# Optimization experiments

Measured on AMD Instinct MI355X. Metric: run time of the kernel, lower is better.

Reference implementation:

```python
import jax, jax.numpy as jnp
import numpy as np

B, N, D_IN, D_EMB = 8, 2048, 768, 768

def setup_inputs() -> dict:
    key = jax.random.key(0)
    k1, k2, k3, k4 = jax.random.split(key, 4)
    x = jax.random.normal(k1, (B, N, D_IN), dtype=jnp.float32)
    # nn.Linear weights stored as [out, in]; applied as x @ W.T
    Wq = jax.random.normal(k2, (D_EMB, D_IN), dtype=jnp.float32) * (D_IN ** -0.5)
    Wk = jax.random.normal(k3, (D_EMB, D_IN), dtype=jnp.float32) * (D_IN ** -0.5)
    Wv = jax.random.normal(k4, (D_EMB, D_IN), dtype=jnp.float32) * (D_IN ** -0.5)
    return {"x": x, "Wq": Wq, "Wk": Wk, "Wv": Wv}

def reference(x, Wq, Wk, Wv):
    dim_sqrt = jnp.asarray(D_EMB ** 0.5, x.dtype)
    q = jnp.einsum('bnd,ed->bne', x, Wq)  # [B,N,E]
    k = jnp.einsum('bnd,ed->bne', x, Wk)
    v = jnp.einsum('bnd,ed->bne', x, Wv)
    scores = jnp.einsum('bne,bme->bnm', q, k)  # [B,N,N]
    # NOTE: module applies softmax FIRST, then divides by sqrt(d) (post-hoc)
    attn = jax.nn.softmax(scores, axis=-1) / dim_sqrt
    out = jnp.einsum('bnm,bme->bne', attn, v)
    return out
```

## Files before the change

### kernel.cpp

```cpp
#include <hip/hip_runtime.h>
#include <stdint.h>
#include <type_traits>

typedef __bf16 bf16;
typedef _Float16 f16;
typedef bf16 bf16x8 __attribute__((ext_vector_type(8)));
typedef f16 f16x8 __attribute__((ext_vector_type(8)));
typedef float f32x4 __attribute__((ext_vector_type(4)));

#define LOG2E 1.4426950408889634f
#define SQRT_E 27.712812921102035f

constexpr int BM = 128, BN = 128, BK = 64;
enum { EPI_F32 = 0, EPI_PAIR = 1, EPI_VT = 2, EPI_F16 = 3 };

__device__ __forceinline__ void async16(const void* g, void* l) {
  __builtin_amdgcn_global_load_lds(
      (__attribute__((address_space(1))) void*)(uintptr_t)g,
      (__attribute__((address_space(3))) void*)l, 16, 0, 0);
}

__device__ __forceinline__ f32x4 mfma8(bf16x8 a, bf16x8 b, f32x4 c) {
  return __builtin_amdgcn_mfma_f32_16x16x32_bf16(a, b, c, 0, 0, 0);
}
__device__ __forceinline__ f32x4 mfma8(f16x8 a, f16x8 b, f32x4 c) {
  return __builtin_amdgcn_mfma_f32_16x16x32_f16(a, b, c, 0, 0, 0);
}

template <typename T, typename TO, int AT, int BT, int EPI, int SWZ>
__global__ __launch_bounds__(256)
void gemm_kernel(const T* __restrict__ Ah, const T* __restrict__ Al,
                 const T* __restrict__ Bh, const T* __restrict__ Bl,
                 void* __restrict__ C0, void* __restrict__ C1,
                 int K, long lda, long ldb, long ldbl, long ldc,
                 long stA, long stB, long stBl, long stC,
                 int gxN, int gyM) {
  using vec8 = typename std::conditional<std::is_same<T, bf16>::value,
                                         bf16x8, f16x8>::type;
  __shared__ __align__(16) T sAh[BM * BK];
  __shared__ __align__(16) T sBh[BN * BK];
  __shared__ __align__(16) T sAl[AT == 2 ? BM * BK : 8];
  __shared__ __align__(16) T sBl[BT == 2 ? BN * BK : 8];

  int bxi, byi, z;
  if constexpr (SWZ) {
    const int id = blockIdx.x;
    const int xcd = id & 7;
    const int j = id >> 3;
    const int s = j / gxN;
    const int n = j - s * gxN;
    const int g = xcd + 8 * s;
    bxi = n;
    byi = g % gyM;
    z = g / gyM;
  } else {
    bxi = blockIdx.x; byi = blockIdx.y; z = blockIdx.z;
  }

  const T* pAh = Ah + (long)z * stA;
  const T* pBh = Bh + (long)z * stB;
  const T* pAl = (AT == 2) ? (Al + (long)z * stA) : nullptr;
  const T* pBl = (BT == 2) ? (Bl + (long)z * stBl) : nullptr;

  const int bm = byi * BM;
  const int bn = bxi * BN;
  const int tid = threadIdx.x;
  const int wave = tid >> 6;
  const int lane = tid & 63;
  const int wm = (wave & 1) * 64;
  const int wn = (wave >> 1) * 64;
  const int quad = lane >> 4;
  const int l16 = lane & 15;

  f32x4 acc[4][4] = {};

  const int sr0 = tid >> 3;
  const int swc = ((tid & 7) ^ (sr0 & 7)) * 8;
  const int cs0 = (quad * 8) ^ ((l16 & 7) << 3);

  for (int kt = 0; kt < K; kt += BK) {
    __syncthreads();
    {
      const long ka = kt + swc;
#pragma unroll
      for (int l = 0; l < 4; ++l) {
        const int row = l * 32 + sr0;
        async16(pAh + (long)(bm + row) * lda + ka, &sAh[(l * 256 + tid) * 8]);
      }
#pragma unroll
      for (int l = 0; l < 4; ++l) {
        const int row = l * 32 + sr0;
        async16(pBh + (long)(bn + row) * ldb + ka, &sBh[(l * 256 + tid) * 8]);
      }
      if constexpr (AT == 2) {
#pragma unroll
        for (int l = 0; l < 4; ++l) {
          const int row = l * 32 + sr0;
          async16(pAl + (long)(bm + row) * lda + ka, &sAl[(l * 256 + tid) * 8]);
        }
      }
      if constexpr (BT == 2) {
#pragma unroll
        for (int l = 0; l < 4; ++l) {
          const int row = l * 32 + sr0;
          async16(pBl + (long)(bn + row) * ldbl + ka, &sBl[(l * 256 + tid) * 8]);
        }
      }
    }
    __syncthreads();

#pragma unroll
    for (int kk = 0; kk < 2; ++kk) {
      const int cs = cs0 ^ (kk * 32);
      vec8 ah[4], al[4];
#pragma unroll
      for (int i = 0; i < 4; ++i) {
        ah[i] = *(const vec8*)&sAh[(wm + i * 16 + l16) * BK + cs];
        if constexpr (AT == 2)
          al[i] = *(const vec8*)&sAl[(wm + i * 16 + l16) * BK + cs];
      }
#pragma unroll
      for (int j = 0; j < 4; ++j) {
        const vec8 bh = *(const vec8*)&sBh[(wn + j * 16 + l16) * BK + cs];
        vec8 bl;
        if constexpr (BT == 2)
          bl = *(const vec8*)&sBl[(wn + j * 16 + l16) * BK + cs];
#pragma unroll
        for (int i = 0; i < 4; ++i) {
          acc[i][j] = mfma8(ah[i], bh, acc[i][j]);
          if constexpr (BT == 2) acc[i][j] = mfma8(ah[i], bl, acc[i][j]);
          if constexpr (AT == 2) acc[i][j] = mfma8(al[i], bh, acc[i][j]);
        }
      }
    }
  }

  if constexpr (EPI == EPI_F32) {
    float* C = (float*)C0 + (long)z * stC;
#pragma unroll
    for (int i = 0; i < 4; ++i) {
      const int mb = bm + wm + i * 16 + quad * 4;
#pragma unroll
      for (int j = 0; j < 4; ++j) {
        const int n = bn + wn + j * 16 + l16;
#pragma unroll
        for (int r = 0; r < 4; ++r)
          C[(long)(mb + r) * ldc + n] = acc[i][j][r];
      }
    }
  } else if constexpr (EPI == EPI_PAIR) {
    TO* Ch = (TO*)C0;
    TO* Cl = (TO*)C1;
#pragma unroll
    for (int i = 0; i < 4; ++i) {
      const int mb = bm + wm + i * 16 + quad * 4;
#pragma unroll
      for (int j = 0; j < 4; ++j) {
        const int n = bn + wn + j * 16 + l16;
#pragma unroll
        for (int r = 0; r < 4; ++r) {
          const float f = acc[i][j][r];
          const TO h = (TO)f;
          const long idx = (long)(mb + r) * ldc + n;
          Ch[idx] = h;
          Cl[idx] = (TO)(f - (float)h);
        }
      }
    }
  } else if constexpr (EPI == EPI_F16) {
    TO* Ch = (TO*)C0;
#pragma unroll
    for (int i = 0; i < 4; ++i) {
      const int mb = bm + wm + i * 16 + quad * 4;
#pragma unroll
      for (int j = 0; j < 4; ++j) {
        const int n = bn + wn + j * 16 + l16;
#pragma unroll
        for (int r = 0; r < 4; ++r)
          Ch[(long)(mb + r) * ldc + n] = (TO)acc[i][j][r];
      }
    }
  } else {
    TO* vT = (TO*)C0;
#pragma unroll
    for (int i = 0; i < 4; ++i) {
      const int mb = bm + wm + i * 16 + quad * 4;
      const long bb = mb >> 11;
      const long ml = mb & 2047;
#pragma unroll
      for (int j = 0; j < 4; ++j) {
        const int e = bn + wn + j * 16 + l16;
        union { TO b[4]; uint2 u; } P;
#pragma unroll
        for (int r = 0; r < 4; ++r) P.b[r] = (TO)acc[i][j][r];
        *(uint2*)&vT[(bb * 768 + e) * 2048 + ml] = P.u;
      }
    }
  }
}

__global__ __launch_bounds__(256)
void softmax_kernel(float* __restrict__ sc) {
  __shared__ float red[4];
  float* srow = sc + (long)blockIdx.x * 2048;
  const int tid = threadIdx.x;
  const int wave = tid >> 6;
  const int lane = tid & 63;
  const float4 v0 = *(const float4*)(srow + tid * 4);
  const float4 v1 = *(const float4*)(srow + 1024 + tid * 4);
  float mx = fmaxf(fmaxf(fmaxf(v0.x, v0.y), fmaxf(v0.z, v0.w)),
                   fmaxf(fmaxf(v1.x, v1.y), fmaxf(v1.z, v1.w)));
#pragma unroll
  for (int o = 32; o >= 1; o >>= 1) mx = fmaxf(mx, __shfl_xor(mx, o));
  if (lane == 0) red[wave] = mx;
  __syncthreads();
  mx = fmaxf(fmaxf(red[0], red[1]), fmaxf(red[2], red[3]));
  const float e0 = exp2f((v0.x - mx) * LOG2E);
  const float e1 = exp2f((v0.y - mx) * LOG2E);
  const float e2 = exp2f((v0.z - mx) * LOG2E);
  const float e3 = exp2f((v0.w - mx) * LOG2E);
  const float e4 = exp2f((v1.x - mx) * LOG2E);
  const float e5 = exp2f((v1.y - mx) * LOG2E);
  const float e6 = exp2f((v1.z - mx) * LOG2E);
  const float e7 = exp2f((v1.w - mx) * LOG2E);
  float s = ((e0 + e1) + (e2 + e3)) + ((e4 + e5) + (e6 + e7));
#pragma unroll
  for (int o = 32; o >= 1; o >>= 1) s += __shfl_xor(s, o);
  __syncthreads();
  if (lane == 0) red[wave] = s;
  __syncthreads();
  s = red[0] + red[1] + red[2] + red[3];
  const float inv = 1.0f / (s * SQRT_E);
  f16* prow = (f16*)srow;
  union { f16 b[4]; uint2 u; } P;
  P.b[0] = (f16)(e0 * inv); P.b[1] = (f16)(e1 * inv);
  P.b[2] = (f16)(e2 * inv); P.b[3] = (f16)(e3 * inv);
  *(uint2*)(prow + tid * 4) = P.u;
  P.b[0] = (f16)(e4 * inv); P.b[1] = (f16)(e5 * inv);
  P.b[2] = (f16)(e6 * inv); P.b[3] = (f16)(e7 * inv);
  *(uint2*)(prow + 1024 + tid * 4) = P.u;
}

__global__ __launch_bounds__(256)
void split_all(const float4* __restrict__ x, const float4* __restrict__ wv,
               uint2* __restrict__ xh, uint2* __restrict__ xl,
               uint2* __restrict__ wvh) {
  constexpr int NX = 3145728;
  constexpr int NWV = 147456;
  const int i = blockIdx.x * 256 + threadIdx.x;
  float4 v;
  uint2 *dh, *dl;
  if (i < NX) {
    v = x[i]; dh = xh + i; dl = xl + i;
  } else {
    const int m = i - NX;
    if (m >= NWV) return;
    v = wv[m]; dh = wvh + m; dl = nullptr;
  }
  const f16 h0 = (f16)v.x, h1 = (f16)v.y, h2 = (f16)v.z, h3 = (f16)v.w;
  union { f16 b[4]; uint2 u; } P;
  P.b[0] = h0; P.b[1] = h1; P.b[2] = h2; P.b[3] = h3;
  *dh = P.u;
  if (dl != nullptr) {
    P.b[0] = (f16)(v.x - (float)h0);
    P.b[1] = (f16)(v.y - (float)h1);
    P.b[2] = (f16)(v.z - (float)h2);
    P.b[3] = (f16)(v.w - (float)h3);
    *dl = P.u;
  }
}

__global__ __launch_bounds__(256)
void transpose_split(const float* __restrict__ Wq, const float* __restrict__ Wk,
                     f16* __restrict__ qTh, f16* __restrict__ qTl,
                     f16* __restrict__ kTh, f16* __restrict__ kTl) {
  __shared__ float tile[64][65];
  const float* src = blockIdx.z ? Wk : Wq;
  f16* dh = blockIdx.z ? kTh : qTh;
  f16* dl = blockIdx.z ? kTl : qTl;
  const int e0 = blockIdx.y * 64, d0 = blockIdx.x * 64;
  const int t = threadIdx.x;
  const int r = t >> 2;
  const int c4 = (t & 3) * 16;
  const float4* s4 = (const float4*)(src + (long)(e0 + r) * 768 + d0 + c4);
#pragma unroll
  for (int g = 0; g < 4; ++g) {
    const float4 v = s4[g];
    tile[r][c4 + g * 4 + 0] = v.x;
    tile[r][c4 + g * 4 + 1] = v.y;
    tile[r][c4 + g * 4 + 2] = v.z;
    tile[r][c4 + g * 4 + 3] = v.w;
  }
  __syncthreads();
  union { f16 b[8]; uint4 u; } H0, H1, L0, L1;
#pragma unroll
  for (int i = 0; i < 16; ++i) {
    const float v = tile[c4 + i][r];
    const f16 h = (f16)v;
    const f16 l = (f16)(v - (float)h);
    if (i < 8) { H0.b[i] = h; L0.b[i] = l; }
    else       { H1.b[i - 8] = h; L1.b[i - 8] = l; }
  }
  const long o = (long)(d0 + r) * 768 + e0 + c4;
  *(uint4*)(dh + o) = H0.u;  *(uint4*)(dh + o + 8) = H1.u;
  *(uint4*)(dl + o) = L0.u;  *(uint4*)(dl + o + 8) = L1.u;
}

extern "C" void kernel_launch(void* const* d_in, const int* in_sizes, int n_in,
                              void* d_out, int out_size, void* d_ws, size_t ws_size,
                              hipStream_t stream) {
  const float* x  = (const float*)d_in[0];
  const float* Wq = (const float*)d_in[1];
  const float* Wk = (const float*)d_in[2];
  const float* Wv = (const float*)d_in[3];
  float* out = (float*)d_out;
  char* ws = (char*)d_ws;

  const size_t SZ = 25165824;
  f16* yh = (f16*)(ws + 0 * SZ);
  f16* xh = (f16*)(ws + 2 * SZ);
  f16* vT = (f16*)(ws + 3 * SZ);
  const size_t PERS = 4 * SZ;
  const size_t WT = 1179648;
  f16* xl   = (f16*)(ws + PERS);
  f16* wqTh = (f16*)(ws + PERS + SZ);
  f16* wqTl = (f16*)(ws + PERS + SZ + 1 * WT);
  f16* wkTh = (f16*)(ws + PERS + SZ + 2 * WT);
  f16* wkTl = (f16*)(ws + PERS + SZ + 3 * WT);
  f16* mtH  = (f16*)(ws + PERS + SZ + 4 * WT);
  f16* mtL  = (f16*)(ws + PERS + SZ + 5 * WT);
  f16* wvh  = (f16*)(ws + PERS + SZ + 6 * WT);
  float* scores = (float*)(ws + PERS);

  long avail = (long)ws_size - (long)PERS;
  int nb = (int)(avail / 16777216);
  if (nb < 1) nb = 1;
  if (nb > 8) nb = 8;

  split_all<<<12864, 256, 0, stream>>>(
      (const float4*)x, (const float4*)Wv, (uint2*)xh, (uint2*)xl, (uint2*)wvh);
  transpose_split<<<dim3(12, 12, 2), 256, 0, stream>>>(
      Wq, Wk, wqTh, wqTl, wkTh, wkTl);

  gemm_kernel<f16, f16, 2, 2, EPI_PAIR, 0><<<dim3(6, 6, 1), 256, 0, stream>>>(
      wkTh, wkTl, wqTh, wqTl, (void*)mtH, (void*)mtL,
      768, 768, 768, 768, 768, 0, 0, 0, 0, 0, 0);

  gemm_kernel<f16, f16, 2, 1, EPI_F16, 1><<<768, 256, 0, stream>>>(
      xh, xl, mtH, nullptr, (void*)yh, nullptr,
      768, 768, 768, 0, 768, 0, 0, 0, 0, 6, 128);

  gemm_kernel<f16, f16, 1, 1, EPI_VT, 1><<<768, 256, 0, stream>>>(
      xh, nullptr, wvh, nullptr, (void*)vT, nullptr,
      768, 768, 768, 0, 0, 0, 0, 0, 0, 6, 128);

  const long RS = 1572864;
  const long VTS = 1572864;
  for (int b0 = 0; b0 < 8; b0 += nb) {
    const int nbg = (8 - b0 < nb) ? (8 - b0) : nb;
    gemm_kernel<f16, float, 1, 1, EPI_F32, 1><<<256 * nbg, 256, 0, stream>>>(
        yh + (long)b0 * RS, nullptr, xh + (long)b0 * RS, nullptr,
        (void*)scores, nullptr,
        768, 768, 768, 0, 2048, RS, RS, 0, 4194304L, 16, 16);
    softmax_kernel<<<nbg * 2048, 256, 0, stream>>>(scores);
    gemm_kernel<f16, float, 1, 1, EPI_F32, 1><<<96 * nbg, 256, 0, stream>>>(
        (const f16*)scores, nullptr, vT + (long)b0 * VTS, nullptr,
        (void*)(out + (long)b0 * 1572864), nullptr,
        2048, 4096, 2048, 0, 768, 8388608L, VTS, 0, 1572864L, 6, 16);
  }
}
```

Baseline: 370.1 us.

## Add double-buffered pipelined GEMM kernel with larger tiles for attention stages

Introduces a new gemm_pipe kernel that double-buffers LDS tiles, issuing async global-to-LDS loads for the next K-tile while computing the current one, with explicit vmcnt waits, MFMA priority hints and an XCD-aware block mapping. The score GEMM moves to 256x256 tiles with 512 threads, and the projection GEMMs use the pipelined path, one of them with BK=32. The goal is to hide global load latency and raise reuse per tile. In exchange it doubles LDS use, which may lower occupancy, and it relies on hand-tuned waitcnt logic.

```diff
diff --git a/kernel.cpp b/kernel.cpp
--- a/kernel.cpp
+++ b/kernel.cpp
@@ -11,7 +11,6 @@
 #define LOG2E 1.4426950408889634f
 #define SQRT_E 27.712812921102035f
 
-constexpr int BM = 128, BN = 128, BK = 64;
 enum { EPI_F32 = 0, EPI_PAIR = 1, EPI_VT = 2, EPI_F16 = 3 };
 
 __device__ __forceinline__ void async16(const void* g, void* l) {
@@ -26,6 +25,199 @@
 __device__ __forceinline__ f32x4 mfma8(f16x8 a, f16x8 b, f32x4 c) {
   return __builtin_amdgcn_mfma_f32_16x16x32_f16(a, b, c, 0, 0, 0);
 }
+
+template <int N>
+__device__ __forceinline__ void vwait() {
+  asm volatile("s_waitcnt vmcnt(%0)" ::"i"(N) : "memory");
+}
+__device__ __forceinline__ void block_bar() {
+  asm volatile("" ::: "memory");
+  __builtin_amdgcn_s_barrier();
+  asm volatile("" ::: "memory");
+}
+
+template <typename T, typename TO, int BMt, int BNt, int BKt, int AT, int EPI>
+__global__ __launch_bounds__((BMt == 256 ? 512 : 256), 2)
+void gemm_pipe(const T* __restrict__ Ah, const T* __restrict__ Al,
+               const T* __restrict__ Bh, void* __restrict__ C0,
+               int K, long lda, long ldb, long ldc,
+               long stA, long stB, long stC, int gxN, int gyM) {
+  using vec8 = typename std::conditional<std::is_same<T, bf16>::value,
+                                         bf16x8, f16x8>::type;
+  static_assert(BMt == BNt, "square tiles only");
+  constexpr int THREADS = (BMt == 256) ? 512 : 256;
+  constexpr int NWN = (BMt == 256) ? 4 : 2;
+  constexpr int WTM = BMt / 2;
+  constexpr int WTN = BNt / NWN;
+  static_assert(WTN == 64, "wave tile must be 64 wide");
+  constexpr int MF = WTM / 16;
+  constexpr int KK = BKt / 32;
+  constexpr int CPR = BKt / 8;
+  constexpr int RPI = THREADS / CPR;
+  constexpr int LPP = (BMt * BKt) / (THREADS * 8);
+  constexpr int LPT = LPP * (AT == 2 ? 3 : 2);
+
+  __shared__ __align__(16) T sA[2][BMt * BKt];
+  __shared__ __align__(16) T sB[2][BNt * BKt];
+  __shared__ __align__(16) T sAl[AT == 2 ? 2 * BMt * BKt : 8];
+
+  const int id = blockIdx.x;
+  const int xcd = id & 7;
+  const int j0 = id >> 3;
+  const int s = j0 / gxN;
+  const int bxi = j0 - s * gxN;
+  const int g = xcd + 8 * s;
+  const int byi = g % gyM;
+  const int z = g / gyM;
+
+  const T* pA = Ah + (long)z * stA;
+  const T* pB = Bh + (long)z * stB;
+  const T* pAl = (AT == 2) ? Al : nullptr;
+
+  const int bm = byi * BMt;
+  const int bn = bxi * BNt;
+  const int tid = threadIdx.x;
+  const int wave = tid >> 6;
+  const int lane = tid & 63;
+  const int wm = (wave / NWN) * WTM;
+  const int wn = (wave % NWN) * WTN;
+  const int quad = lane >> 4;
+  const int l16 = lane & 15;
+
+  f32x4 acc[MF][4] = {};
+
+  const int srow = tid / CPR;
+  const int schk = tid % CPR;
+  const int swc = ((BKt == 64) ? (schk ^ (srow & 7)) : schk) * 8;
+  const int cs0 = (quad * 8) ^ ((BKt == 64) ? ((l16 & 7) << 3) : 0);
+
+  const int NT = K / BKt;
+
+  auto stage = [&](int buf, int t) {
+    const long ka = (long)t * BKt + swc;
+#pragma unroll
+    for (int l = 0; l < LPP; ++l)
+      async16(pA + (long)(bm + l * RPI + srow) * lda + ka,
+              &sA[buf][(l * THREADS + tid) * 8]);
+#pragma unroll
+    for (int l = 0; l < LPP; ++l)
+      async16(pB + (long)(bn + l * RPI + srow) * ldb + ka,
+              &sB[buf][(l * THREADS + tid) * 8]);
+    if constexpr (AT == 2) {
+#pragma unroll
+      for (int l = 0; l < LPP; ++l)
+        async16(pAl + (long)(bm + l * RPI + srow) * lda + ka,
+                &sAl[buf * BMt * BKt + (l * THREADS + tid) * 8]);
+    }
+  };
+
+  auto compute = [&](int buf) {
+    const T* bA = &sA[buf][0];
+    const T* bB = &sB[buf][0];
+    const T* bAl = (AT == 2) ? &sAl[buf * BMt * BKt] : nullptr;
+    vec8 bf[KK][4];
+#pragma unroll
+    for (int kk = 0; kk < KK; ++kk)
+#pragma unroll
+      for (int jj = 0; jj < 4; ++jj)
+        bf[kk][jj] =
+            *(const vec8*)&bB[(wn + jj * 16 + l16) * BKt + (cs0 ^ (kk * 32))];
+#pragma unroll
+    for (int mq = 0; mq < MF / 2; ++mq) {
+      vec8 af[KK][2];
+      vec8 alf[AT == 2 ? KK : 1][2];
+#pragma unroll
+      for (int kk = 0; kk < KK; ++kk)
+#pragma unroll
+        for (int ii = 0; ii < 2; ++ii) {
+          const int r = wm + mq * 32 + ii * 16 + l16;
+          af[kk][ii] = *(const vec8*)&bA[r * BKt + (cs0 ^ (kk * 32))];
+          if constexpr (AT == 2)
+            alf[kk][ii] = *(const vec8*)&bAl[r * BKt + (cs0 ^ (kk * 32))];
+        }
+      __builtin_amdgcn_s_setprio(1);
+#pragma unroll
+      for (int jj = 0; jj < 4; ++jj)
+#pragma unroll
+        for (int ii = 0; ii < 2; ++ii)
+#pragma unroll
+          for (int kk = 0; kk < KK; ++kk) {
+            acc[mq * 2 + ii][jj] =
+                mfma8(af[kk][ii], bf[kk][jj], acc[mq * 2 + ii][jj]);
+            if constexpr (AT == 2)
+              acc[mq * 2 + ii][jj] =
+                  mfma8(alf[kk][ii], bf[kk][jj], acc[mq * 2 + ii][jj]);
+          }
+      __builtin_amdgcn_s_setprio(0);
+    }
+  };
+
+  stage(0, 0);
+  stage(1, 1);
+  vwait<LPT>();
+  block_bar();
+
+  for (int t = 0; t < NT; ++t) {
+    const int cur = t & 1;
+    compute(cur);
+    if (t + 1 < NT) {
+      block_bar();
+      if (t + 2 < NT) {
+        stage(cur, t + 2);
+        vwait<LPT>();
+      } else {
+        vwait<0>();
+      }
+      block_bar();
+    }
+  }
+
+  if constexpr (EPI == EPI_F32) {
+    float* C = (float*)C0 + (long)z * stC;
+#pragma unroll
+    for (int i = 0; i < MF; ++i) {
+      const int mb = bm + wm + i * 16 + quad * 4;
+#pragma unroll
+      for (int j = 0; j < 4; ++j) {
+        const int n = bn + wn + j * 16 + l16;
+#pragma unroll
+        for (int r = 0; r < 4; ++r)
+          C[(long)(mb + r) * ldc + n] = acc[i][j][r];
+      }
+    }
+  } else if constexpr (EPI == EPI_F16) {
+    TO* Ch = (TO*)C0;
+#pragma unroll
+    for (int i = 0; i < MF; ++i) {
+      const int mb = bm + wm + i * 16 + quad * 4;
+#pragma unroll
+      for (int j = 0; j < 4; ++j) {
+        const int n = bn + wn + j * 16 + l16;
+#pragma unroll
+        for (int r = 0; r < 4; ++r)
+          Ch[(long)(mb + r) * ldc + n] = (TO)acc[i][j][r];
+      }
+    }
+  } else {
+    TO* vT = (TO*)C0;
+#pragma unroll
+    for (int i = 0; i < MF; ++i) {
+      const int mb = bm + wm + i * 16 + quad * 4;
+      const long bb = mb >> 11;
+      const long ml = mb & 2047;
+#pragma unroll
+      for (int j = 0; j < 4; ++j) {
+        const int e = bn + wn + j * 16 + l16;
+        union { TO b[4]; uint2 u; } P;
+#pragma unroll
+        for (int r = 0; r < 4; ++r) P.b[r] = (TO)acc[i][j][r];
+        *(uint2*)&vT[(bb * 768 + e) * 2048 + ml] = P.u;
+      }
+    }
+  }
+}
+
+constexpr int BM = 128, BN = 128, BK = 64;
 
 template <typename T, typename TO, int AT, int BT, int EPI, int SWZ>
 __global__ __launch_bounds__(256)
@@ -135,20 +327,7 @@
     }
   }
 
-  if constexpr (EPI == EPI_F32) {
-    float* C = (float*)C0 + (long)z * stC;
-#pragma unroll
-    for (int i = 0; i < 4; ++i) {
-      const int mb = bm + wm + i * 16 + quad * 4;
-#pragma unroll
-      for (int j = 0; j < 4; ++j) {
-        const int n = bn + wn + j * 16 + l16;
-#pragma unroll
-        for (int r = 0; r < 4; ++r)
-          C[(long)(mb + r) * ldc + n] = acc[i][j][r];
-      }
-    }
-  } else if constexpr (EPI == EPI_PAIR) {
+  if constexpr (EPI == EPI_PAIR) {
     TO* Ch = (TO*)C0;
     TO* Cl = (TO*)C1;
 #pragma unroll
@@ -165,35 +344,6 @@
           Ch[idx] = h;
           Cl[idx] = (TO)(f - (float)h);
         }
-      }
-    }
-  } else if constexpr (EPI == EPI_F16) {
-    TO* Ch = (TO*)C0;
-#pragma unroll
-    for (int i = 0; i < 4; ++i) {
-      const int mb = bm + wm + i * 16 + quad * 4;
-#pragma unroll
-      for (int j = 0; j < 4; ++j) {
-        const int n = bn + wn + j * 16 + l16;
-#pragma unroll
-        for (int r = 0; r < 4; ++r)
-          Ch[(long)(mb + r) * ldc + n] = (TO)acc[i][j][r];
-      }
-    }
-  } else {
-    TO* vT = (TO*)C0;
-#pragma unroll
-    for (int i = 0; i < 4; ++i) {
-      const int mb = bm + wm + i * 16 + quad * 4;
-      const long bb = mb >> 11;
-      const long ml = mb & 2047;
-#pragma unroll
-      for (int j = 0; j < 4; ++j) {
-        const int e = bn + wn + j * 16 + l16;
-        union { TO b[4]; uint2 u; } P;
-#pragma unroll
-        for (int r = 0; r < 4; ++r) P.b[r] = (TO)acc[i][j][r];
-        *(uint2*)&vT[(bb * 768 + e) * 2048 + ml] = P.u;
       }
     }
   }
@@ -346,26 +496,23 @@
       wkTh, wkTl, wqTh, wqTl, (void*)mtH, (void*)mtL,
       768, 768, 768, 768, 768, 0, 0, 0, 0, 0, 0);
 
-  gemm_kernel<f16, f16, 2, 1, EPI_F16, 1><<<768, 256, 0, stream>>>(
-      xh, xl, mtH, nullptr, (void*)yh, nullptr,
-      768, 768, 768, 0, 768, 0, 0, 0, 0, 6, 128);
-
-  gemm_kernel<f16, f16, 1, 1, EPI_VT, 1><<<768, 256, 0, stream>>>(
-      xh, nullptr, wvh, nullptr, (void*)vT, nullptr,
-      768, 768, 768, 0, 0, 0, 0, 0, 0, 6, 128);
+  gemm_pipe<f16, f16, 128, 128, 32, 2, EPI_F16><<<768, 256, 0, stream>>>(
+      xh, xl, mtH, (void*)yh, 768, 768, 768, 768, 0, 0, 0, 6, 128);
+
+  gemm_pipe<f16, f16, 128, 128, 64, 1, EPI_VT><<<768, 256, 0, stream>>>(
+      xh, nullptr, wvh, (void*)vT, 768, 768, 768, 0, 0, 0, 0, 6, 128);
 
   const long RS = 1572864;
   const long VTS = 1572864;
   for (int b0 = 0; b0 < 8; b0 += nb) {
     const int nbg = (8 - b0 < nb) ? (8 - b0) : nb;
-    gemm_kernel<f16, float, 1, 1, EPI_F32, 1><<<256 * nbg, 256, 0, stream>>>(
-        yh + (long)b0 * RS, nullptr, xh + (long)b0 * RS, nullptr,
-        (void*)scores, nullptr,
-        768, 768, 768, 0, 2048, RS, RS, 0, 4194304L, 16, 16);
+    gemm_pipe<f16, float, 256, 256, 64, 1, EPI_F32><<<64 * nbg, 512, 0, stream>>>(
+        yh + (long)b0 * RS, nullptr, xh + (long)b0 * RS, (void*)scores,
+        768, 768, 768, 2048, RS, RS, 4194304L, 8, 8);
     softmax_kernel<<<nbg * 2048, 256, 0, stream>>>(scores);
-    gemm_kernel<f16, float, 1, 1, EPI_F32, 1><<<96 * nbg, 256, 0, stream>>>(
-        (const f16*)scores, nullptr, vT + (long)b0 * VTS, nullptr,
-        (void*)(out + (long)b0 * 1572864), nullptr,
-        2048, 4096, 2048, 0, 768, 8388608L, VTS, 0, 1572864L, 6, 16);
-  }
-}
+    gemm_pipe<f16, float, 128, 128, 64, 1, EPI_F32><<<96 * nbg, 256, 0, stream>>>(
+        (const f16*)scores, nullptr, vT + (long)b0 * VTS,
+        (void*)(out + (long)b0 * 1572864),
+        2048, 4096, 2048, 768, 8388608L, VTS, 1572864L, 6, 16);
+  }
+}
```

New measurement: 376.6 us. About the same (+1.8%).
